# Optimization experiments

Measured on AMD Instinct MI355X. Metric: run time of the kernel, lower is better.

Reference implementation:

```python
import jax, jax.numpy as jnp
import numpy as np

B, N, D, W, IMG = 16384, 20, 64, 64, 2048
NUM_USERS, NUM_ITEMS, NUM_INGRE = 100000, 201000, 33001


def setup_inputs() -> dict:
    key = jax.random.key(0)
    ks = jax.random.split(key, 24)
    s = lambda *sh: 1.0 / np.sqrt(sh[0])
    inp = {
        'user_input': jax.random.randint(ks[0], (B,), 0, NUM_USERS),
        'item_input': jax.random.randint(ks[1], (B,), 0, NUM_ITEMS),
        'ingre_input': jax.random.randint(ks[2], (B, N), 0, NUM_INGRE),
        'image_input': jax.random.normal(ks[3], (B, IMG), dtype=jnp.float32),
        'ingre_num': jax.random.randint(ks[4], (B,), 1, N + 1),
        'user_emb': jax.random.normal(ks[5], (NUM_USERS, D), dtype=jnp.float32) * 0.01,
        'item_emb': jax.random.normal(ks[6], (NUM_ITEMS, D), dtype=jnp.float32) * 0.01,
        'ingre_emb': jax.random.normal(ks[7], (NUM_INGRE, D), dtype=jnp.float32) * 0.01,
        'W_image_w': jax.random.normal(ks[8], (IMG, D), dtype=jnp.float32) * s(IMG),
        'W_image_b': jnp.zeros((D,), jnp.float32),
        'b_image': jnp.zeros((1, D), jnp.float32),
        'W_concat_w': jax.random.normal(ks[9], (3 * D, D), dtype=jnp.float32) * s(3 * D),
        'W_concat_b': jnp.zeros((D,), jnp.float32),
        'b_concat': jnp.zeros((1, D), jnp.float32),
        'h_w': jax.random.normal(ks[10], (D, 1), dtype=jnp.float32) * s(D),
        'h_b': jnp.zeros((1,), jnp.float32),
        'W_att_ingre_w': jax.random.normal(ks[11], (3 * D, W), dtype=jnp.float32) * s(3 * D),
        'W_att_ingre_b': jnp.zeros((W,), jnp.float32),
        'b_att_ingre': jnp.zeros((1, W), jnp.float32),
        'v': jnp.ones((W, 1), jnp.float32),
        'W_att_com_w': jax.random.normal(ks[12], (2 * D, W), dtype=jnp.float32) * s(2 * D),
        'W_att_com_b': jnp.zeros((W,), jnp.float32),
        'b_att_com': jnp.zeros((1, W), jnp.float32),
        'v_c': jnp.ones((W, 1), jnp.float32),
    }
    return inp


def reference(user_input, item_input, ingre_input, image_input, ingre_num,
              user_emb, item_emb, ingre_emb,
              W_image_w, W_image_b, b_image,
              W_concat_w, W_concat_b, b_concat, h_w, h_b,
              W_att_ingre_w, W_att_ingre_b, b_att_ingre, v,
              W_att_com_w, W_att_com_b, b_att_com, v_c):
    b = user_input.shape[0]
    ue = user_emb[user_input]                       # [B, D]
    ie = item_emb[item_input]                       # [B, D]
    qe = ingre_emb[ingre_input]                     # [B, N, D]
    img = image_input @ W_image_w + W_image_b + b_image  # [B, D]

    # ---- ingredient-level attention ----
    n = qe.shape[1]
    tile_p = jnp.broadcast_to(ue[:, None, :], (b, n, ue.shape[-1]))
    tile_i = jnp.broadcast_to(img[:, None, :], (b, n, img.shape[-1]))
    concat_v = jnp.concatenate([qe, tile_p, tile_i], axis=2)     # [B, N, 3D]
    mlp = jnp.tanh(concat_v @ W_att_ingre_w + W_att_ingre_b + b_att_ingre[0])  # [B, N, W]
    A_ = (mlp @ v)[..., 0]                                        # [B, N]
    mask = (jnp.arange(n)[None, :] < ingre_num[:, None]).astype(A_.dtype)
    A_ = A_ * mask + (1.0 - mask) * (-1e12)
    A = jax.nn.softmax(A_, axis=1)[..., None]                     # [B, N, 1]
    ingre_att = jnp.sum(A * qe, axis=1)                           # [B, D]

    # ---- component-level attention (faithful to original cat+view order) ----
    cp = jnp.concatenate([
        jnp.concatenate([ue, ie], axis=1),
        jnp.concatenate([ue, ingre_att], axis=1),
        jnp.concatenate([ue, img], axis=1),
    ], axis=0)                                                    # [3B, 2D]
    ch = jnp.tanh(cp @ W_att_com_w + W_att_com_b + b_att_com[0])  # [3B, W]
    scores = (ch @ v_c).reshape(b, -1)                            # [B, 3] (row-major, as torch .view)
    Bw = jax.nn.softmax(scores, axis=1)[..., None]                # [B, 3, 1]
    ce = jnp.stack([ie, ingre_att, img], axis=1)                  # [B, 3, D]
    item_att = jnp.sum(Bw * ce, axis=1)                           # [B, D]

    # ---- prediction head ----
    uic = jnp.concatenate([ue, item_att, ue * item_att], axis=-1) # [B, 3D]
    hidden = jax.nn.relu(uic @ W_concat_w + W_concat_b + b_concat[0])
    out = hidden @ h_w + h_b                                      # [B, 1]
    return out
```

## Files before the change

### kernel.cpp

```cpp
#include <hip/hip_runtime.h>
#include <hip/hip_fp16.h>

#define BB 16384
#define NN 20
#define DD 64
#define IMGK 2048

using bf16x8 = __attribute__((ext_vector_type(8))) short;
using f32x4  = __attribute__((ext_vector_type(4))) float;

typedef __attribute__((address_space(1))) const unsigned int GUint;
typedef __attribute__((address_space(3))) unsigned int LUint;
__device__ __forceinline__ void gl_lds16(const void* g, void* l) {
  __builtin_amdgcn_global_load_lds((GUint*)g, (LUint*)l, 16, 0, 0);
}

__device__ __forceinline__ float waveReduceSum(float x) {
#pragma unroll
  for (int off = 32; off > 0; off >>= 1) x += __shfl_xor(x, off, 64);
  return x;
}

__device__ __forceinline__ float fast_tanh(float x) {
  float e = __expf(2.f * x);
  return 1.f - __fdividef(2.f, e + 1.f);
}

__device__ __forceinline__ short f2bf(float f) {
  union { float f; unsigned u; } c; c.f = f;
  unsigned r = c.u + 0x7fffu + ((c.u >> 16) & 1u);
  return (short)(r >> 16);
}
__device__ __forceinline__ float bf2f(short s) {
  union { unsigned u; float f; } c; c.u = ((unsigned)(unsigned short)s) << 16;
  return c.f;
}

__device__ __forceinline__ unsigned pack_hi(float a, float b) {
  unsigned ua = __float_as_uint(a), ub = __float_as_uint(b);
  return (ub & 0xffff0000u) | (ua >> 16);
}
__device__ __forceinline__ float trunc_bf(float a) {
  return __uint_as_float(__float_as_uint(a) & 0xffff0000u);
}

__global__ __launch_bounds__(256)
void prep_kernel(const float* __restrict__ Wimg, const float* __restrict__ W1,
                 const float* __restrict__ Wc,
                 short* __restrict__ Wf, short* __restrict__ W1f,
                 short* __restrict__ Wcf) {
  int i = blockIdx.x * 256 + threadIdx.x;
  if (i < 32768) {
    const int lane = i & 63;
    const int h = (i >> 6) & 1;
    const int tt = (i >> 7) & 3;
    const int ks = (i >> 9) & 1;
    const int kq = i >> 10;
    const int n = 16 * tt + (lane & 15);
    const int kb = kq * 64 + ks * 32 + (lane >> 4) * 8;
    union { short s[8]; bf16x8 v; } o;
#pragma unroll
    for (int j = 0; j < 8; ++j) {
      float f = Wimg[(size_t)(kb + j) * 64 + n];
      short hi = f2bf(f);
      o.s[j] = h == 0 ? hi : f2bf(f - bf2f(hi));
    }
    reinterpret_cast<bf16x8*>(Wf)[i] = o.v;
  } else if (i < 32768 + 1536) {
    const int j = i - 32768;
    const int lane = j & 63;
    const int wt = (j >> 6) & 3;
    const int ks = j >> 8;
    const int n = 16 * wt + (lane & 15);
    const int kb = ks * 32 + (lane >> 4) * 8;
    union { short s[8]; bf16x8 v; } o;
#pragma unroll
    for (int jj = 0; jj < 8; ++jj)
      o.s[jj] = f2bf(W1[(size_t)(kb + jj) * 64 + n]);
    reinterpret_cast<bf16x8*>(W1f)[j] = o.v;
  } else if (i < 32768 + 1536 + 1024) {
    const int j = i - 32768 - 1536;
    const int lane = j & 63;
    const int wt = (j >> 6) & 3;
    const int ks = j >> 8;
    const int n = 16 * wt + (lane & 15);
    const int kb = ks * 32 + (lane >> 4) * 8;
    union { short s[8]; bf16x8 v; } o;
#pragma unroll
    for (int jj = 0; jj < 8; ++jj)
      o.s[jj] = f2bf(Wc[(size_t)(kb + jj) * 64 + n]);
    reinterpret_cast<bf16x8*>(Wcf)[j] = o.v;
  }
}

__global__ __launch_bounds__(256, 5)
void img_gemm_mfma(const float* __restrict__ img_in,
                   const short* __restrict__ Wf,
                   __half* __restrict__ pp) {
  __shared__ short wlds[8192];
  __shared__ float alds[4096];
  const int t = threadIdx.x;
  const int wave = t >> 6, lane = t & 63;
  const int lr = lane & 15, lk = lane >> 4;
  const int kq = blockIdx.x & 31, rgb = blockIdx.x >> 5;
  const int r0 = rgb * 64;
  __half* pout = pp + (size_t)kq * BB * 64;

  const short* wsrc = Wf + (size_t)kq * 8192;
#pragma unroll
  for (int i = 0; i < 4; ++i) {
    int j = i * 256 + t;
    gl_lds16(wsrc + j * 8, wlds + j * 8);
  }
#pragma unroll
  for (int i = 0; i < 4; ++i) {
    int j = i * 256 + t;
    int r = j >> 4, c = j & 15;
    int gc = (c ^ (r & 7)) * 4;
    gl_lds16(img_in + (size_t)(r0 + r) * IMGK + kq * 64 + gc, alds + j * 4);
  }
  asm volatile("s_waitcnt vmcnt(0)" ::: "memory");
  __syncthreads();

  const int arow = wave * 16 + lr;
  const int rx = arow & 7;
  float4 Af[2][2];
#pragma unroll
  for (int ks = 0; ks < 2; ++ks) {
    const int s0 = ks * 8 + lk * 2;
    Af[ks][0] = *reinterpret_cast<const float4*>(alds + arow * 64 + (s0 ^ rx) * 4);
    Af[ks][1] = *reinterpret_cast<const float4*>(alds + arow * 64 + ((s0 + 1) ^ rx) * 4);
  }
  const bf16x8* wp = reinterpret_cast<const bf16x8*>(wlds);
  f32x4 aHH[4], aER[4];
#pragma unroll
  for (int tt = 0; tt < 4; ++tt) {
    aHH[tt] = (f32x4){0.f, 0.f, 0.f, 0.f};
    aER[tt] = (f32x4){0.f, 0.f, 0.f, 0.f};
  }
#pragma unroll
  for (int ks = 0; ks < 2; ++ks) {
    float4 va = Af[ks][0], vb = Af[ks][1];
    union { unsigned u[4]; bf16x8 v; } hi, lo;
    hi.u[0] = pack_hi(va.x, va.y);
    hi.u[1] = pack_hi(va.z, va.w);
    hi.u[2] = pack_hi(vb.x, vb.y);
    hi.u[3] = pack_hi(vb.z, vb.w);
    lo.u[0] = pack_hi(va.x - trunc_bf(va.x), va.y - trunc_bf(va.y));
    lo.u[1] = pack_hi(va.z - trunc_bf(va.z), va.w - trunc_bf(va.w));
    lo.u[2] = pack_hi(vb.x - trunc_bf(vb.x), vb.y - trunc_bf(vb.y));
    lo.u[3] = pack_hi(vb.z - trunc_bf(vb.z), vb.w - trunc_bf(vb.w));
#pragma unroll
    for (int tt = 0; tt < 4; ++tt) {
      bf16x8 wh = wp[((ks * 4 + tt) * 2 + 0) * 64 + lane];
      bf16x8 wl = wp[((ks * 4 + tt) * 2 + 1) * 64 + lane];
      aHH[tt] = __builtin_amdgcn_mfma_f32_16x16x32_bf16(hi.v, wh, aHH[tt], 0, 0, 0);
      aER[tt] = __builtin_amdgcn_mfma_f32_16x16x32_bf16(hi.v, wl, aER[tt], 0, 0, 0);
      aER[tt] = __builtin_amdgcn_mfma_f32_16x16x32_bf16(lo.v, wh, aER[tt], 0, 0, 0);
    }
  }
#pragma unroll
  for (int tt = 0; tt < 4; ++tt)
#pragma unroll
    for (int r = 0; r < 4; ++r)
      alds[(size_t)(wave * 16 + 4 * lk + r) * 64 + 16 * tt + lr] = aHH[tt][r] + aER[tt][r];
  asm volatile("s_waitcnt lgkmcnt(0)" ::: "memory");
  {
    const int row_l = lane >> 2, colq = (lane & 3) * 16;
    const float* src = alds + (size_t)(wave * 16 + row_l) * 64 + colq;
    union { __half h[8]; int4 v; } o1, o2;
#pragma unroll
    for (int j = 0; j < 8; ++j) {
      o1.h[j] = __float2half(src[j]);
      o2.h[j] = __float2half(src[8 + j]);
    }
    __half* dst = pout + (size_t)(r0 + wave * 16 + row_l) * 64 + colq;
    *reinterpret_cast<int4*>(dst) = o1.v;
    *reinterpret_cast<int4*>(dst + 8) = o2.v;
  }
}

__global__ __launch_bounds__(256)
void img_combine(const __half* __restrict__ pp,
                 const float* __restrict__ Wb, const float* __restrict__ bimg,
                 float* __restrict__ ws_img) {
  const int i = blockIdx.x * 256 + threadIdx.x;
  const int e = i * 2;
  const int col = e & 63;
  float2 wb = *reinterpret_cast<const float2*>(&Wb[col]);
  float2 bi = *reinterpret_cast<const float2*>(&bimg[col]);
  float2 s;
  s.x = wb.x + bi.x;
  s.y = wb.y + bi.y;
#pragma unroll
  for (int kq = 0; kq < 32; ++kq) {
    __half2 h = *reinterpret_cast<const __half2*>(pp + (size_t)kq * BB * 64 + e);
    float2 f = __half22float2(h);
    s.x += f.x;
    s.y += f.y;
  }
  *reinterpret_cast<float2*>(ws_img + e) = s;
}

__global__ __launch_bounds__(256, 3)
void mid_kernel(const int* __restrict__ user_input,
                const int* __restrict__ item_input,
                const int* __restrict__ ingre_input,
                const int* __restrict__ ingre_num,
                const float* __restrict__ user_emb,
                const float* __restrict__ item_emb,
                const float* __restrict__ ingre_emb,
                const short* __restrict__ W1f,
                const float* __restrict__ Wib, const float* __restrict__ bai,
                const float* __restrict__ v,
                const short* __restrict__ Wcf,
                const float* __restrict__ Wcb, const float* __restrict__ bac,
                const float* __restrict__ vc,
                const float* __restrict__ ws_img,
                float* __restrict__ ws_ia,
                float* __restrict__ ws_flat) {
  __shared__ short wflds[12288];
  __shared__ short qe_s[4][32][88];
  __shared__ short ui_s[4][256];
  __shared__ float P4_s[4][4][64];
  __shared__ float sc_s[4][32];
  const int t = threadIdx.x;
  const int wave = t >> 6, lane = t & 63;
  const int lr = lane & 15, lk = lane >> 4;
  const int b = blockIdx.x * 4 + wave;

  for (int i = t; i < 1536; i += 256)
    reinterpret_cast<bf16x8*>(wflds)[i] = reinterpret_cast<const bf16x8*>(W1f)[i];

  float qv[NN];
#pragma unroll
  for (int n = 0; n < NN; ++n) {
    const int gi = ingre_input[b * NN + n];
    qv[n] = ingre_emb[(size_t)gi * 64 + lane];
  }
  const float s = ws_img[(size_t)b * 64 + lane];
  const int u = user_input[b];
  const int it = item_input[b];
  const float ue = user_emb[(size_t)u * 64 + lane];
  const float iev = item_emb[(size_t)it * 64 + lane];
  float vv[4], biasw[4];
#pragma unroll
  for (int wt = 0; wt < 4; ++wt) {
    vv[wt] = v[16 * wt + lr];
    biasw[wt] = Wib[16 * wt + lr] + bai[16 * wt + lr];
  }
  const float bbc = Wcb[lane] + bac[lane];
  const float vcl = vc[lane];

#pragma unroll
  for (int n = 0; n < NN; ++n) qe_s[wave][n][lane] = f2bf(qv[n]);
#pragma unroll
  for (int n = NN; n < 32; ++n) qe_s[wave][n][lane] = 0;
  ui_s[wave][lane] = f2bf(ue);
  ui_s[wave][64 + lane] = f2bf(s);
  ui_s[wave][128 + lane] = f2bf(iev);
  __syncthreads();

  bf16x8 aq0[2], aq1[2], au[4];
#pragma unroll
  for (int ks = 0; ks < 2; ++ks) {
    aq0[ks] = *reinterpret_cast<const bf16x8*>(&qe_s[wave][lr][ks * 32 + lk * 8]);
    aq1[ks] = *reinterpret_cast<const bf16x8*>(&qe_s[wave][16 + lr][ks * 32 + lk * 8]);
  }
#pragma unroll
  for (int ks = 0; ks < 4; ++ks)
    au[ks] = *reinterpret_cast<const bf16x8*>(&ui_s[wave][ks * 32 + lk * 8]);

  const bf16x8* wp = reinterpret_cast<const bf16x8*>(wflds);
  f32x4 accq[2][4], accb[4];
#pragma unroll
  for (int wt = 0; wt < 4; ++wt) {
    accq[0][wt] = (f32x4){0.f, 0.f, 0.f, 0.f};
    accq[1][wt] = (f32x4){0.f, 0.f, 0.f, 0.f};
    accb[wt] = (f32x4){0.f, 0.f, 0.f, 0.f};
  }
#pragma unroll
  for (int ks = 0; ks < 2; ++ks)
#pragma unroll
    for (int wt = 0; wt < 4; ++wt) {
      bf16x8 w = wp[(ks * 4 + wt) * 64 + lane];
      accq[0][wt] = __builtin_amdgcn_mfma_f32_16x16x32_bf16(aq0[ks], w, accq[0][wt], 0, 0, 0);
      accq[1][wt] = __builtin_amdgcn_mfma_f32_16x16x32_bf16(aq1[ks], w, accq[1][wt], 0, 0, 0);
    }
#pragma unroll
  for (int ks = 2; ks < 6; ++ks)
#pragma unroll
    for (int wt = 0; wt < 4; ++wt) {
      bf16x8 w = wp[(ks * 4 + wt) * 64 + lane];
      accb[wt] = __builtin_amdgcn_mfma_f32_16x16x32_bf16(au[ks - 2], w, accb[wt], 0, 0, 0);
    }
  float basew[4];
#pragma unroll
  for (int wt = 0; wt < 4; ++wt) basew[wt] = accb[wt][0] + biasw[wt];

  float sp[2][4];
#pragma unroll
  for (int nt = 0; nt < 2; ++nt)
#pragma unroll
    for (int r = 0; r < 4; ++r) {
      float sv = 0.f;
#pragma unroll
      for (int wt = 0; wt < 4; ++wt) {
        float x = accq[nt][wt][r] + basew[wt];
        sv = fmaf(fast_tanh(x), vv[wt], sv);
      }
      sp[nt][r] = sv;
    }
#pragma unroll
  for (int off = 1; off < 16; off <<= 1)
#pragma unroll
    for (int nt = 0; nt < 2; ++nt)
#pragma unroll
      for (int r = 0; r < 4; ++r) sp[nt][r] += __shfl_xor(sp[nt][r], off, 64);
  if (lr == 0) {
#pragma unroll
    for (int r = 0; r < 4; ++r) {
      sc_s[wave][4 * lk + r] = sp[0][r];
      sc_s[wave][16 + 4 * lk + r] = sp[1][r];
    }
  }
  asm volatile("s_waitcnt lgkmcnt(0)" ::: "memory");
  float scn[NN];
#pragma unroll
  for (int q = 0; q < 5; ++q) {
    float4 s4 = *reinterpret_cast<const float4*>(&sc_s[wave][4 * q]);
    scn[4 * q + 0] = s4.x; scn[4 * q + 1] = s4.y;
    scn[4 * q + 2] = s4.z; scn[4 * q + 3] = s4.w;
  }
  asm volatile("s_waitcnt lgkmcnt(0)" ::: "memory");
  const int num = ingre_num[b];
  float m = -3e38f;
#pragma unroll
  for (int n = 0; n < NN; ++n) {
    scn[n] = (n < num) ? scn[n] : -1e12f;
    m = fmaxf(m, scn[n]);
  }
  float ssum = 0.f;
#pragma unroll
  for (int n = 0; n < NN; ++n) {
    scn[n] = __expf(scn[n] - m);
    ssum += scn[n];
  }
  const float inv = __fdividef(1.f, ssum);
  float ia = 0.f;
#pragma unroll
  for (int n = 0; n < NN; ++n) ia = fmaf(scn[n], qv[n], ia);
  ia *= inv;
  ws_ia[(size_t)b * 64 + lane] = ia;

  ui_s[wave][192 + lane] = f2bf(ia);
  asm volatile("s_waitcnt lgkmcnt(0)" ::: "memory");
  const bf16x8 zerov = (bf16x8){0, 0, 0, 0, 0, 0, 0, 0};
  f32x4 accU[4], accY[4];
#pragma unroll
  for (int wt = 0; wt < 4; ++wt) {
    accU[wt] = (f32x4){0.f, 0.f, 0.f, 0.f};
    accY[wt] = (f32x4){0.f, 0.f, 0.f, 0.f};
  }
  const int yoff = (lr == 0) ? 128 : (lr == 1) ? 192 : 64;
#pragma unroll
  for (int ks = 0; ks < 2; ++ks) {
    bf16x8 aU = (lr == 0)
        ? *reinterpret_cast<const bf16x8*>(&ui_s[wave][ks * 32 + lk * 8]) : zerov;
    bf16x8 aY = (lr < 3)
        ? *reinterpret_cast<const bf16x8*>(&ui_s[wave][yoff + ks * 32 + lk * 8]) : zerov;
#pragma unroll
    for (int wt = 0; wt < 4; ++wt) {
      bf16x8 wU = *reinterpret_cast<const bf16x8*>(Wcf + ((ks * 4 + wt) * 64 + lane) * 8);
      bf16x8 wY = *reinterpret_cast<const bf16x8*>(Wcf + (((ks + 2) * 4 + wt) * 64 + lane) * 8);
      accU[wt] = __builtin_amdgcn_mfma_f32_16x16x32_bf16(aU, wU, accU[wt], 0, 0, 0);
      accY[wt] = __builtin_amdgcn_mfma_f32_16x16x32_bf16(aY, wY, accY[wt], 0, 0, 0);
    }
  }
  if (lk == 0) {
#pragma unroll
    for (int wt = 0; wt < 4; ++wt) {
      P4_s[wave][0][wt * 16 + lr] = accU[wt][0];
      P4_s[wave][1][wt * 16 + lr] = accY[wt][0];
      P4_s[wave][2][wt * 16 + lr] = accY[wt][1];
      P4_s[wave][3][wt * 16 + lr] = accY[wt][2];
    }
  }
  asm volatile("s_waitcnt lgkmcnt(0)" ::: "memory");
  const float su = P4_s[wave][0][lane] + bbc;
  float sc3[3];
#pragma unroll
  for (int c = 0; c < 3; ++c) {
    float x = su + P4_s[wave][1 + c][lane];
    sc3[c] = waveReduceSum(fast_tanh(x) * vcl);
  }
  if (lane == 0) {
    ws_flat[b] = sc3[0];
    ws_flat[BB + b] = sc3[1];
    ws_flat[2 * BB + b] = sc3[2];
  }
}

__global__ __launch_bounds__(256, 3)
void head_kernel(const int* __restrict__ user_input,
                 const int* __restrict__ item_input,
                 const float* __restrict__ user_emb,
                 const float* __restrict__ item_emb,
                 const float* __restrict__ Wcat,
                 const float* __restrict__ Wcatb,
                 const float* __restrict__ bcat,
                 const float* __restrict__ hw,
                 const float* __restrict__ hb,
                 const float* __restrict__ ws_img,
                 const float* __restrict__ ws_ia,
                 const float* __restrict__ ws_flat,
                 float* __restrict__ out) {
  __shared__ float Wlds[192 * 64];
  __shared__ float ue_s[4][64];
  __shared__ float itt_s[4][64];
  const int t = threadIdx.x;
  for (int i = t; i < 192 * 64 / 4; i += 256)
    reinterpret_cast<float4*>(Wlds)[i] = reinterpret_cast<const float4*>(Wcat)[i];
  __syncthreads();
  const int wave = t >> 6, lane = t & 63;
  const float bb = Wcatb[lane] + bcat[lane];
  const float hwl = hw[lane];
  const float hbv = hb[0];
  const int b0 = blockIdx.x * 16 + wave * 4;
#pragma unroll 1
  for (int bi = 0; bi < 4; ++bi) {
    const int b = b0 + bi;
    const float s0 = ws_flat[3 * b + 0];
    const float s1 = ws_flat[3 * b + 1];
    const float s2 = ws_flat[3 * b + 2];
    const float m = fmaxf(s0, fmaxf(s1, s2));
    const float e0 = __expf(s0 - m), e1 = __expf(s1 - m), e2 = __expf(s2 - m);
    const float inv = 1.0f / (e0 + e1 + e2);
    const int u = user_input[b];
    const int it = item_input[b];
    const float uev = user_emb[(size_t)u * 64 + lane];
    const float itt = (e0 * item_emb[(size_t)it * 64 + lane] +
                       e1 * ws_ia[(size_t)b * 64 + lane] +
                       e2 * ws_img[(size_t)b * 64 + lane]) * inv;
    ue_s[wave][lane] = uev;
    itt_s[wave][lane] = itt;
    asm volatile("s_waitcnt lgkmcnt(0)" ::: "memory");
    const float4* u4 = reinterpret_cast<const float4*>(&ue_s[wave][0]);
    const float4* i4 = reinterpret_cast<const float4*>(&itt_s[wave][0]);
    float h = bb;
#pragma unroll
    for (int d0 = 0; d0 < 16; ++d0) {
      float4 uu = u4[d0];
      float4 ii = i4[d0];
      int d = d0 * 4;
      h = fmaf(uu.x, Wlds[(d + 0) * 64 + lane], h);
      h = fmaf(ii.x, Wlds[(64 + d + 0) * 64 + lane], h);
      h = fmaf(uu.x * ii.x, Wlds[(128 + d + 0) * 64 + lane], h);
      h = fmaf(uu.y, Wlds[(d + 1) * 64 + lane], h);
      h = fmaf(ii.y, Wlds[(64 + d + 1) * 64 + lane], h);
      h = fmaf(uu.y * ii.y, Wlds[(128 + d + 1) * 64 + lane], h);
      h = fmaf(uu.z, Wlds[(d + 2) * 64 + lane], h);
      h = fmaf(ii.z, Wlds[(64 + d + 2) * 64 + lane], h);
      h = fmaf(uu.z * ii.z, Wlds[(128 + d + 2) * 64 + lane], h);
      h = fmaf(uu.w, Wlds[(d + 3) * 64 + lane], h);
      h = fmaf(ii.w, Wlds[(64 + d + 3) * 64 + lane], h);
      h = fmaf(uu.w * ii.w, Wlds[(128 + d + 3) * 64 + lane], h);
    }
    h = fmaxf(h, 0.f) * hwl;
    float o = waveReduceSum(h);
    if (lane == 0) out[b] = o + hbv;
    asm volatile("s_waitcnt lgkmcnt(0)" ::: "memory");
  }
}

extern "C" void kernel_launch(void* const* d_in, const int* in_sizes, int n_in,
                              void* d_out, int out_size, void* d_ws, size_t ws_size,
                              hipStream_t stream) {
  (void)in_sizes; (void)n_in; (void)out_size; (void)ws_size;
  const int* user_input = (const int*)d_in[0];
  const int* item_input = (const int*)d_in[1];
  const int* ingre_input = (const int*)d_in[2];
  const float* image_input = (const float*)d_in[3];
  const int* ingre_num = (const int*)d_in[4];
  const float* user_emb = (const float*)d_in[5];
  const float* item_emb = (const float*)d_in[6];
  const float* ingre_emb = (const float*)d_in[7];
  const float* W_image_w = (const float*)d_in[8];
  const float* W_image_b = (const float*)d_in[9];
  const float* b_image = (const float*)d_in[10];
  const float* W_concat_w = (const float*)d_in[11];
  const float* W_concat_b = (const float*)d_in[12];
  const float* b_concat = (const float*)d_in[13];
  const float* h_w = (const float*)d_in[14];
  const float* h_b = (const float*)d_in[15];
  const float* W_att_ingre_w = (const float*)d_in[16];
  const float* W_att_ingre_b = (const float*)d_in[17];
  const float* b_att_ingre = (const float*)d_in[18];
  const float* v = (const float*)d_in[19];
  const float* W_att_com_w = (const float*)d_in[20];
  const float* W_att_com_b = (const float*)d_in[21];
  const float* b_att_com = (const float*)d_in[22];
  const float* v_c = (const float*)d_in[23];

  float* ws = (float*)d_ws;
  float* ws_img = ws;
  float* ws_ia = ws + (size_t)BB * 64;
  float* ws_flat = ws + (size_t)2 * BB * 64;
  short* Wf = (short*)(ws + (size_t)2 * BB * 64 + 3 * BB);
  short* W1f = Wf + (size_t)32 * 8192;
  short* Wcf = W1f + 12288;
  __half* pp = (__half*)(Wcf + 8192);
  float* out = (float*)d_out;

  prep_kernel<<<(32768 + 1536 + 1024 + 255) / 256, 256, 0, stream>>>(
      W_image_w, W_att_ingre_w, W_att_com_w, Wf, W1f, Wcf);
  img_gemm_mfma<<<8192, 256, 0, stream>>>(image_input, Wf, pp);
  img_combine<<<BB * 64 / 2 / 256, 256, 0, stream>>>(pp, W_image_b, b_image, ws_img);
  mid_kernel<<<BB / 4, 256, 0, stream>>>(user_input, item_input, ingre_input, ingre_num,
                                         user_emb, item_emb, ingre_emb,
                                         W1f, W_att_ingre_b, b_att_ingre, v,
                                         Wcf, W_att_com_b, b_att_com, v_c,
                                         ws_img, ws_ia, ws_flat);
  head_kernel<<<BB / 16, 256, 0, stream>>>(user_input, item_input, user_emb, item_emb,
                                           W_concat_w, W_concat_b, b_concat, h_w, h_b,
                                           ws_img, ws_ia, ws_flat, out);
}
```

Before: 134.9 us.

## Load ingredient embeddings and W1 weights directly into LDS via global_load_lds

Ingredient embedding rows and the W1f weight tile now go straight from global memory into LDS through global_load_lds, so they no longer pass through VGPRs. The ingredient index row is loaded once per wave and broadcast with shuffles, and ingre_num is loaded earlier. qe_s now holds fp32, is converted to bf16 when the MFMA operands are read, and is re-read from LDS for the weighted sum. This lowers register pressure and removes the per-row register staging and padding stores, at the cost of more LDS space and extra LDS reads.

```diff
diff --git a/kernel.cpp b/kernel.cpp
--- a/kernel.cpp
+++ b/kernel.cpp
@@ -14,6 +14,9 @@
 __device__ __forceinline__ void gl_lds16(const void* g, void* l) {
   __builtin_amdgcn_global_load_lds((GUint*)g, (LUint*)l, 16, 0, 0);
 }
+__device__ __forceinline__ void gl_lds4(const void* g, void* l) {
+  __builtin_amdgcn_global_load_lds((GUint*)g, (LUint*)l, 4, 0, 0);
+}
 
 __device__ __forceinline__ float waveReduceSum(float x) {
 #pragma unroll
@@ -34,6 +37,13 @@
 __device__ __forceinline__ float bf2f(short s) {
   union { unsigned u; float f; } c; c.u = ((unsigned)(unsigned short)s) << 16;
   return c.f;
+}
+
+__device__ __forceinline__ bf16x8 pack8_rne(float4 a, float4 b) {
+  union { short s[8]; bf16x8 v; } r;
+  r.s[0] = f2bf(a.x); r.s[1] = f2bf(a.y); r.s[2] = f2bf(a.z); r.s[3] = f2bf(a.w);
+  r.s[4] = f2bf(b.x); r.s[5] = f2bf(b.y); r.s[6] = f2bf(b.z); r.s[7] = f2bf(b.w);
+  return r.v;
 }
 
 __device__ __forceinline__ unsigned pack_hi(float a, float b) {
@@ -220,7 +230,7 @@
                 float* __restrict__ ws_ia,
                 float* __restrict__ ws_flat) {
   __shared__ short wflds[12288];
-  __shared__ short qe_s[4][32][88];
+  __shared__ float qe_s[4][NN][68];
   __shared__ short ui_s[4][256];
   __shared__ float P4_s[4][4][64];
   __shared__ float sc_s[4][32];
@@ -229,20 +239,23 @@
   const int lr = lane & 15, lk = lane >> 4;
   const int b = blockIdx.x * 4 + wave;
 
-  for (int i = t; i < 1536; i += 256)
-    reinterpret_cast<bf16x8*>(wflds)[i] = reinterpret_cast<const bf16x8*>(W1f)[i];
-
-  float qv[NN];
+#pragma unroll
+  for (int i = 0; i < 6; ++i) {
+    const int g = i * 256 + wave * 64;
+    gl_lds16(W1f + (size_t)(g + lane) * 8, wflds + (size_t)g * 8);
+  }
+  const int gidx = ingre_input[b * NN + ((lane < NN) ? lane : (NN - 1))];
 #pragma unroll
   for (int n = 0; n < NN; ++n) {
-    const int gi = ingre_input[b * NN + n];
-    qv[n] = ingre_emb[(size_t)gi * 64 + lane];
+    const int gi = __shfl(gidx, n, 64);
+    gl_lds4(ingre_emb + (size_t)gi * 64 + lane, &qe_s[wave][n][0]);
   }
   const float s = ws_img[(size_t)b * 64 + lane];
   const int u = user_input[b];
   const int it = item_input[b];
   const float ue = user_emb[(size_t)u * 64 + lane];
   const float iev = item_emb[(size_t)it * 64 + lane];
+  const int num = ingre_num[b];
   float vv[4], biasw[4];
 #pragma unroll
   for (int wt = 0; wt < 4; ++wt) {
@@ -252,20 +265,22 @@
   const float bbc = Wcb[lane] + bac[lane];
   const float vcl = vc[lane];
 
-#pragma unroll
-  for (int n = 0; n < NN; ++n) qe_s[wave][n][lane] = f2bf(qv[n]);
-#pragma unroll
-  for (int n = NN; n < 32; ++n) qe_s[wave][n][lane] = 0;
   ui_s[wave][lane] = f2bf(ue);
   ui_s[wave][64 + lane] = f2bf(s);
   ui_s[wave][128 + lane] = f2bf(iev);
+  asm volatile("s_waitcnt vmcnt(0)" ::: "memory");
   __syncthreads();
 
+  const int r1 = (16 + lr < NN) ? 16 + lr : 0;
   bf16x8 aq0[2], aq1[2], au[4];
 #pragma unroll
   for (int ks = 0; ks < 2; ++ks) {
-    aq0[ks] = *reinterpret_cast<const bf16x8*>(&qe_s[wave][lr][ks * 32 + lk * 8]);
-    aq1[ks] = *reinterpret_cast<const bf16x8*>(&qe_s[wave][16 + lr][ks * 32 + lk * 8]);
+    const float* p0 = &qe_s[wave][lr][ks * 32 + lk * 8];
+    aq0[ks] = pack8_rne(*reinterpret_cast<const float4*>(p0),
+                        *reinterpret_cast<const float4*>(p0 + 4));
+    const float* p1 = &qe_s[wave][r1][ks * 32 + lk * 8];
+    aq1[ks] = pack8_rne(*reinterpret_cast<const float4*>(p1),
+                        *reinterpret_cast<const float4*>(p1 + 4));
   }
 #pragma unroll
   for (int ks = 0; ks < 4; ++ks)
@@ -333,7 +348,6 @@
     scn[4 * q + 2] = s4.z; scn[4 * q + 3] = s4.w;
   }
   asm volatile("s_waitcnt lgkmcnt(0)" ::: "memory");
-  const int num = ingre_num[b];
   float m = -3e38f;
 #pragma unroll
   for (int n = 0; n < NN; ++n) {
@@ -349,7 +363,7 @@
   const float inv = __fdividef(1.f, ssum);
   float ia = 0.f;
 #pragma unroll
-  for (int n = 0; n < NN; ++n) ia = fmaf(scn[n], qv[n], ia);
+  for (int n = 0; n < NN; ++n) ia = fmaf(scn[n], qe_s[wave][n][lane], ia);
   ia *= inv;
   ws_ia[(size_t)b * 64 + lane] = ia;
 
```

New measurement: 139.7 us. +3.6%, slower.
